# Kernel optimization log

Hardware: AMD Instinct MI355X
Metric: run time of the kernel (lower is better)

Reference implementation:

```python
import jax, jax.numpy as jnp
import numpy as np

D_MODEL = 1024
N_HEADS = 16
D_K = D_MODEL // N_HEADS
D_FF = 4096
EPS = 1e-5


def setup_inputs() -> dict:
    key = jax.random.key(0)
    ks = jax.random.split(key, 12)
    s = 1.0 / np.sqrt(D_MODEL)
    inp = {
        "x": jax.random.normal(ks[0], (2, 2048, D_MODEL), dtype=jnp.float32),
        "Wq": jax.random.normal(ks[1], (D_MODEL, D_MODEL), dtype=jnp.float32) * s,
        "Wk": jax.random.normal(ks[2], (D_MODEL, D_MODEL), dtype=jnp.float32) * s,
        "Wv": jax.random.normal(ks[3], (D_MODEL, D_MODEL), dtype=jnp.float32) * s,
        "Wo": jax.random.normal(ks[4], (D_MODEL, D_MODEL), dtype=jnp.float32) * s,
        "ln1_g": jnp.ones((D_MODEL,), jnp.float32),
        "ln1_b": jnp.zeros((D_MODEL,), jnp.float32),
        "ln2_g": jnp.ones((D_MODEL,), jnp.float32),
        "ln2_b": jnp.zeros((D_MODEL,), jnp.float32),
        "W1": jax.random.normal(ks[5], (D_MODEL, D_FF), dtype=jnp.float32) * s,
        "b1": jnp.zeros((D_FF,), jnp.float32),
        "W2": jax.random.normal(ks[6], (D_FF, D_MODEL), dtype=jnp.float32) * (1.0 / np.sqrt(D_FF)),
        "b2": jnp.zeros((D_MODEL,), jnp.float32),
    }
    return inp


def _layernorm(x, g, b):
    mu = jnp.mean(x, axis=-1, keepdims=True)
    var = jnp.mean(jnp.square(x - mu), axis=-1, keepdims=True)
    return (x - mu) / jnp.sqrt(var + EPS) * g + b


def _mha(x, Wq, Wk, Wv, Wo):
    B, S, D = x.shape
    def split_heads(t):
        return t.reshape(B, S, N_HEADS, D_K).transpose(0, 2, 1, 3)  # [B,H,S,Dk]
    Q = split_heads(x @ Wq)
    K = split_heads(x @ Wk)
    V = split_heads(x @ Wv)
    scores = jnp.einsum("bhsd,bhtd->bhst", Q, K) / np.sqrt(D_K)
    causal = jnp.tril(jnp.ones((S, S), dtype=bool))
    scores = jnp.where(causal, scores, -jnp.inf)
    weights = jax.nn.softmax(scores, axis=-1)
    out = jnp.einsum("bhst,bhtd->bhsd", weights, V)
    out = out.transpose(0, 2, 1, 3).reshape(B, S, D)
    return out @ Wo


def reference(x, Wq, Wk, Wv, Wo, ln1_g, ln1_b, ln2_g, ln2_b, W1, b1, W2, b2):
    # Pre-LN transformer block, dropout in eval mode (identity)
    x = x + _mha(_layernorm(x, ln1_g, ln1_b), Wq, Wk, Wv, Wo)
    h = _layernorm(x, ln2_g, ln2_b)
    ff = jax.nn.gelu(h @ W1 + b1, approximate=False) @ W2 + b2
    return x + ff
```

## Files before the change

kernel.cpp:

```cpp
#include <hip/hip_runtime.h>
#include <cstdint>
#include <cstddef>

#define DEV __device__ __forceinline__

typedef __attribute__((ext_vector_type(8))) __bf16 bf16x8;
typedef __attribute__((ext_vector_type(4))) float f32x4;
typedef __attribute__((ext_vector_type(8))) unsigned short u16x8;

typedef const __attribute__((address_space(1))) void gld_gv;
typedef __attribute__((address_space(3))) void gld_sv;

static constexpr int SEQ = 2048, BAT = 2, DM = 1024, DFF = 4096;
static constexpr int MT = BAT * SEQ;
static constexpr float LOG2E = 1.44269504088896340736f;
static constexpr float SM_SHIFT = 16.0f;

struct TrueC  { static constexpr bool value = true;  };
struct FalseC { static constexpr bool value = false; };

DEV unsigned short f2bf_bits(float f) {
    uint32_t u = __builtin_bit_cast(uint32_t, f);
    return (unsigned short)((u + 0x7FFFu + ((u >> 16) & 1u)) >> 16);
}

DEV void gload16(const void* g, void* s) {
    __builtin_amdgcn_global_load_lds((gld_gv*)g, (gld_sv*)s, 16, 0, 0);
}

__global__ __launch_bounds__(256) void wtrans_kernel(const float* __restrict__ W,
        unsigned short* __restrict__ WT, int K, int N, float scale)
{
    __shared__ float tile[64][65];
    const int k0 = blockIdx.x * 64, n0 = blockIdx.y * 64;
    const int t = threadIdx.x, r = t >> 6, c = t & 63;
    #pragma unroll
    for (int p = 0; p < 16; ++p)
        tile[p * 4 + r][c] = W[(size_t)(k0 + p * 4 + r) * N + n0 + c];
    __syncthreads();
    #pragma unroll
    for (int p = 0; p < 16; ++p)
        WT[(size_t)(n0 + p * 4 + r) * K + k0 + c] = f2bf_bits(tile[c][p * 4 + r] * scale);
}

__global__ __launch_bounds__(256) void ln_kernel(const float* __restrict__ x,
        const float* __restrict__ gw, const float* __restrict__ bw,
        unsigned short* __restrict__ y)
{
    const int row = blockIdx.x, t = threadIdx.x;
    const float* xr = x + (size_t)row * DM;
    float4 v = *(const float4*)(xr + t * 4);
    float s = v.x + v.y + v.z + v.w;
    float q = v.x * v.x + v.y * v.y + v.z * v.z + v.w * v.w;
    #pragma unroll
    for (int m = 1; m < 64; m <<= 1) { s += __shfl_xor(s, m); q += __shfl_xor(q, m); }
    __shared__ float red[8];
    const int w = t >> 6;
    if ((t & 63) == 0) { red[w] = s; red[4 + w] = q; }
    __syncthreads();
    s = red[0] + red[1] + red[2] + red[3];
    q = red[4] + red[5] + red[6] + red[7];
    const float mu = s * (1.0f / DM);
    const float rstd = rsqrtf(q * (1.0f / DM) - mu * mu + 1e-5f);
    float4 g4 = *(const float4*)(gw + t * 4);
    float4 b4 = *(const float4*)(bw + t * 4);
    short4 o;
    o.x = (short)f2bf_bits((v.x - mu) * rstd * g4.x + b4.x);
    o.y = (short)f2bf_bits((v.y - mu) * rstd * g4.y + b4.y);
    o.z = (short)f2bf_bits((v.z - mu) * rstd * g4.z + b4.z);
    o.w = (short)f2bf_bits((v.w - mu) * rstd * g4.w + b4.w);
    *(short4*)(y + (size_t)row * DM + t * 4) = o;
}

template<int EPI, int BM, int BN, int WVM, int WVN>
__global__ __launch_bounds__(WVM * WVN * 64, (BN == 64 ? 3 : 2)) void gemm_pipe(
    const unsigned short* __restrict__ A, const unsigned short* __restrict__ BT,
    void* __restrict__ Cp, const float* __restrict__ bias,
    const float* __restrict__ res, int Nsz, int Ksz, float scale)
{
    constexpr int NT = WVM * WVN * 64;
    constexpr int TOTCH = (BM + BN) * 8;
    constexpr int TL = TOTCH / NT;
    constexpr int MREP = BM / (WVM * 16);
    constexpr int WMR = MREP * 16;
    __shared__ alignas(16) unsigned short lds[2][(BM + BN) * 64];

    const int t = threadIdx.x, l = t & 63, w = t >> 6;
    const int wm = w / WVN, wn = w % WVN;
    const int lr = l & 15, lg = l >> 4;
    const int bm = blockIdx.x, bn = blockIdx.y;

    f32x4 acc[MREP][4] = {};

    const int nk = Ksz / 64;

    auto STAGE = [&](int tile, char* slot) {
        const int k0 = tile * 64;
        #pragma unroll
        for (int p = 0; p < TL; ++p) {
            const int ci = t + p * NT;
            const bool isA = ci < BM * 8;
            const int rr = (isA ? ci : ci - BM * 8) >> 3;
            const int cc = ci & 7;
            const unsigned short* srow = isA
                ? A + (size_t)(bm * BM + rr) * Ksz
                : BT + (size_t)(bn * BN + rr) * Ksz;
            gload16(srow + k0 + ((cc ^ (rr & 7)) << 3), slot + ci * 16);
        }
    };

    STAGE(0, (char*)lds[0]);
    STAGE(1, (char*)lds[1]);

    for (int kt = 0; kt < nk; ++kt) {
        char* slot = (char*)lds[kt & 1];
        const char* la = slot;
        const char* lb = slot + BM * 128;
        if (kt + 1 < nk) {
            if constexpr (TL == 8) asm volatile("s_waitcnt vmcnt(8)" ::: "memory");
            else                   asm volatile("s_waitcnt vmcnt(6)" ::: "memory");
        } else {
            asm volatile("s_waitcnt vmcnt(0)" ::: "memory");
        }
        __builtin_amdgcn_s_barrier();
        __builtin_amdgcn_sched_barrier(0);

        __builtin_amdgcn_s_setprio(1);
        #pragma unroll
        for (int ks = 0; ks < 2; ++ks) {
            bf16x8 af[MREP], bfr[4];
            #pragma unroll
            for (int i = 0; i < MREP; ++i) {
                const int ra = wm * WMR + i * 16 + lr;
                af[i] = *(const bf16x8*)(la + (ra * 8 + ((ks * 4 + lg) ^ (ra & 7))) * 16);
            }
            #pragma unroll
            for (int i = 0; i < 4; ++i) {
                const int rb_ = wn * 64 + i * 16 + lr;
                bfr[i] = *(const bf16x8*)(lb + (rb_ * 8 + ((ks * 4 + lg) ^ (rb_ & 7))) * 16);
            }
            #pragma unroll
            for (int mb = 0; mb < MREP; ++mb)
                #pragma unroll
                for (int nb = 0; nb < 4; ++nb) {
                    if (EPI == 4)
                        acc[mb][nb] = __builtin_amdgcn_mfma_f32_16x16x32_bf16(
                            bfr[nb], af[mb], acc[mb][nb], 0, 0, 0);
                    else
                        acc[mb][nb] = __builtin_amdgcn_mfma_f32_16x16x32_bf16(
                            af[mb], bfr[nb], acc[mb][nb], 0, 0, 0);
                }
        }
        __builtin_amdgcn_s_setprio(0);
        __builtin_amdgcn_s_barrier();
        if (kt + 2 < nk) STAGE(kt + 2, slot);
    }

    const int rb = bm * BM + wm * WMR, cb = bn * BN + wn * 64;
    #pragma unroll
    for (int mb = 0; mb < MREP; ++mb)
        #pragma unroll
        for (int nb = 0; nb < 4; ++nb)
            #pragma unroll
            for (int r = 0; r < 4; ++r) {
                float v = acc[mb][nb][r];
                if (EPI == 4) {
                    const int xrow = rb + mb * 16 + lr;
                    const int feat = cb + nb * 16 + lg * 4 + r;
                    const int bb = xrow >> 11, s = xrow & (SEQ - 1);
                    ((unsigned short*)Cp)[((size_t)bb * DM + feat) * SEQ + s] = f2bf_bits(v);
                    continue;
                }
                const int row = rb + mb * 16 + lg * 4 + r;
                const int col = cb + nb * 16 + lr;
                const size_t idx = (size_t)row * Nsz + col;
                if (EPI == 0) {
                    ((unsigned short*)Cp)[idx] = f2bf_bits(v * scale);
                } else if (EPI == 1) {
                    ((float*)Cp)[idx] = v + res[idx];
                } else if (EPI == 2) {
                    float xx = v + bias[col];
                    ((unsigned short*)Cp)[idx] =
                        f2bf_bits(0.5f * xx * (1.0f + erff(xx * 0.70710678118654752f)));
                } else {
                    ((float*)Cp)[idx] = v + bias[col] + res[idx];
                }
            }
}

template<int P>
DEV void phase8_mfma(const char* base, int wm, int lr, int lg,
                     const bf16x8 (&bfr)[2][4], f32x4 (&acc)[8][4]) {
    bf16x8 af[2][2];
    #pragma unroll
    for (int ks = 0; ks < 2; ++ks)
        #pragma unroll
        for (int m = 0; m < 2; ++m) {
            const int ra = wm * 128 + P * 32 + m * 16 + lr;
            af[ks][m] = *(const bf16x8*)(base + (ra * 8 + ((ks * 4 + lg) ^ (ra & 7))) * 16);
        }
    __builtin_amdgcn_s_barrier();
    __builtin_amdgcn_s_setprio(1);
    #pragma unroll
    for (int ks = 0; ks < 2; ++ks)
        #pragma unroll
        for (int m = 0; m < 2; ++m)
            #pragma unroll
            for (int nb = 0; nb < 4; ++nb)
                acc[P * 2 + m][nb] = __builtin_amdgcn_mfma_f32_16x16x32_bf16(
                    af[ks][m], bfr[ks][nb], acc[P * 2 + m][nb], 0, 0, 0);
    __builtin_amdgcn_s_setprio(0);
}

template<int EPI>
__global__ __launch_bounds__(512, 2) void gemm_8ph(
    const unsigned short* __restrict__ A, const unsigned short* __restrict__ BT,
    void* __restrict__ Cp, const float* __restrict__ bias,
    const float* __restrict__ res, int Nsz, int Ksz, float scale)
{
    __shared__ alignas(16) unsigned short lds[2][32768];
    const int t = threadIdx.x, l = t & 63, w = t >> 6;
    const int wm = w >> 2, wn = w & 3;
    const int lr = l & 15, lg = l >> 4;
    const int bm = blockIdx.x, bn = blockIdx.y;

    f32x4 acc[8][4] = {};
    const int nk = Ksz / 64;

    const unsigned short* Ab = A + (size_t)(bm * 256) * Ksz;
    const unsigned short* Bb = BT + (size_t)(bn * 256) * Ksz;

    auto stage = [&](int tile, int region) {
        char* base = (char*)lds[tile & 1];
        const int k0 = tile * 64;
        #pragma unroll
        for (int j = 0; j < 2; ++j) {
            const int ci = t + j * 512;
            const int rr = ci >> 3, c = ci & 7;
            int row; const unsigned short* src; int dchunk;
            if (region == 0)      { row = rr;                          src = Bb; dchunk = 2048 + row * 8 + c; }
            else if (region == 1) { row = 128 + rr;                    src = Bb; dchunk = 2048 + row * 8 + c; }
            else if (region == 2) { row = (rr < 64 ? rr : rr + 64);    src = Ab; dchunk = row * 8 + c; }
            else                  { row = 64 + (rr < 64 ? rr : rr + 64); src = Ab; dchunk = row * 8 + c; }
            gload16(src + (size_t)row * Ksz + k0 + ((c ^ (row & 7)) << 3),
                    base + dchunk * 16);
        }
    };

    stage(0, 0); stage(0, 1); stage(0, 2); stage(0, 3);
    stage(1, 0); stage(1, 1); stage(1, 2);
    asm volatile("s_waitcnt vmcnt(6)" ::: "memory");
    __builtin_amdgcn_s_barrier();
    __builtin_amdgcn_sched_barrier(0);

    bf16x8 bfr[2][4];
    for (int kt = 0; kt < nk; ++kt) {
        const char* base = (const char*)lds[kt & 1];
        if (kt + 1 < nk) stage(kt + 1, 3);
        #pragma unroll
        for (int ks = 0; ks < 2; ++ks)
            #pragma unroll
            for (int nb = 0; nb < 4; ++nb) {
                const int rb_ = wn * 64 + nb * 16 + lr;
                bfr[ks][nb] = *(const bf16x8*)(base
                    + (2048 + rb_ * 8 + ((ks * 4 + lg) ^ (rb_ & 7))) * 16);
            }
        phase8_mfma<0>(base, wm, lr, lg, bfr, acc);
        __builtin_amdgcn_s_barrier();
        if (kt + 2 < nk) stage(kt + 2, 0);
        phase8_mfma<1>(base, wm, lr, lg, bfr, acc);
        __builtin_amdgcn_s_barrier();
        if (kt + 2 < nk) stage(kt + 2, 1);
        phase8_mfma<2>(base, wm, lr, lg, bfr, acc);
        __builtin_amdgcn_s_barrier();
        if (kt + 2 < nk) stage(kt + 2, 2);
        phase8_mfma<3>(base, wm, lr, lg, bfr, acc);
        if (kt + 2 < nk) asm volatile("s_waitcnt vmcnt(6)" ::: "memory");
        else             asm volatile("s_waitcnt vmcnt(0)" ::: "memory");
        __builtin_amdgcn_s_barrier();
        __builtin_amdgcn_sched_barrier(0);
    }

    const int rb = bm * 256 + wm * 128, cb = bn * 256 + wn * 64;
    #pragma unroll
    for (int mb = 0; mb < 8; ++mb)
        #pragma unroll
        for (int nb = 0; nb < 4; ++nb)
            #pragma unroll
            for (int r = 0; r < 4; ++r) {
                float v = acc[mb][nb][r];
                const int row = rb + mb * 16 + lg * 4 + r;
                const int col = cb + nb * 16 + lr;
                const size_t idx = (size_t)row * Nsz + col;
                if (EPI == 2) {
                    const float xx = v + bias[col];
                    const float tq = xx * xx;
                    const float u = xx * fmaf(tq, 0.044715f, 1.0f);
                    const float e = exp2f(u * -2.30220795f);
                    ((unsigned short*)Cp)[idx] =
                        f2bf_bits(xx * __builtin_amdgcn_rcpf(1.0f + e));
                } else if (EPI == 0) {
                    ((unsigned short*)Cp)[idx] = f2bf_bits(v * scale);
                } else {
                    ((float*)Cp)[idx] = v + bias[col] + res[idx];
                }
            }
}

__global__ __launch_bounds__(512, 2) void attn_kernel(
    const unsigned short* __restrict__ QKg, const unsigned short* __restrict__ VTg,
    unsigned short* __restrict__ Og)
{
    __shared__ alignas(16) unsigned short ldsK[2][128 * 64];
    __shared__ alignas(16) unsigned short ldsVT[2][64 * 128];
    const int t = threadIdx.x, l = t & 63, w = t >> 6;
    const int lr = l & 15, lg = l >> 4;
    const int qtA = blockIdx.x, qtB = 15 - qtA;
    const int bh = blockIdx.y;
    const int b = bh >> 4, h = bh & 15;
    const unsigned short* Qbase = QKg + (size_t)b * SEQ * 2048 + h * 64;
    const unsigned short* Kbase = Qbase + 1024;
    const unsigned short* Vbase = VTg + (size_t)b * DM * SEQ + (size_t)(h * 64) * SEQ;

    const int wq0A = qtA * 128 + w * 16, qrowA = wq0A + lr;
    const int wq0B = qtB * 128 + w * 16, qrowB = wq0B + lr;
    bf16x8 qfA[2], qfB[2];
    #pragma unroll
    for (int ks = 0; ks < 2; ++ks) {
        qfA[ks] = *(const bf16x8*)(Qbase + (size_t)qrowA * 2048 + ks * 32 + lg * 8);
        qfB[ks] = *(const bf16x8*)(Qbase + (size_t)qrowB * 2048 + ks * 32 + lg * 8);
    }

    f32x4 oaccA[4] = {}, oaccB[4] = {};
    f32x4 laccA = {}, laccB = {};
    bf16x8 onesv;
    #pragma unroll
    for (int i = 0; i < 8; ++i) onesv[i] = (__bf16)1.0f;

    const int kci[2] = { t, t + 512 };
    const int nkt = qtB + 1;

    #pragma unroll
    for (int p = 0; p < 2; ++p) {
        const int ci = kci[p];
        const int kr = ci >> 3, kc = (ci & 7) ^ (kr & 7);
        gload16(Kbase + (size_t)kr * 2048 + kc * 8, (char*)ldsK[0] + ci * 16);
        const int vr = ci >> 4, vc = (ci & 15) ^ (vr & 15);
        gload16(Vbase + (size_t)vr * SEQ + vc * 8, (char*)ldsVT[0] + ci * 16);
    }
    asm volatile("s_waitcnt vmcnt(0)" ::: "memory");
    __builtin_amdgcn_s_barrier();

    for (int kt = 0; kt < nkt; ++kt) {
        const int cur = kt & 1;
        if (kt + 1 < nkt) {
            #pragma unroll
            for (int p = 0; p < 2; ++p) {
                const int ci = kci[p];
                const int kr = ci >> 3, kc = (ci & 7) ^ (kr & 7);
                gload16(Kbase + (size_t)((kt + 1) * 128 + kr) * 2048 + kc * 8,
                        (char*)ldsK[cur ^ 1] + ci * 16);
                const int vr = ci >> 4, vc = (ci & 15) ^ (vr & 15);
                gload16(Vbase + (size_t)vr * SEQ + (kt + 1) * 128 + vc * 8,
                        (char*)ldsVT[cur ^ 1] + ci * 16);
            }
        }
        const char* lk = (const char*)ldsK[cur];
        const char* lv = (const char*)ldsVT[cur];
        const int kt0 = kt * 128;

        auto run_softmax = [&](f32x4 (&st)[8], int qrow, bool diag, bf16x8 (&pa)[4]) {
            if (diag) {
                #pragma unroll
                for (int mb = 0; mb < 8; ++mb)
                    #pragma unroll
                    for (int r = 0; r < 4; ++r)
                        if (kt0 + mb * 16 + lg * 4 + r > qrow) st[mb][r] = -1e30f;
            }
            #pragma unroll
            for (int mb = 0; mb < 8; ++mb)
                #pragma unroll
                for (int r = 0; r < 4; ++r)
                    st[mb][r] = exp2f(st[mb][r]);
            #pragma unroll
            for (int ks = 0; ks < 4; ++ks)
                #pragma unroll
                for (int j = 0; j < 4; ++j) {
                    pa[ks][j]     = (__bf16)st[2 * ks][j];
                    pa[ks][j + 4] = (__bf16)st[2 * ks + 1][j];
                }
        };

        auto iter_body = [&](auto DOA) {
            constexpr bool doA = DOA.value;
            f32x4 stA[8], stB[8];
            #pragma unroll
            for (int mb = 0; mb < 8; ++mb)
                #pragma unroll
                for (int r = 0; r < 4; ++r) { stA[mb][r] = -SM_SHIFT; stB[mb][r] = -SM_SHIFT; }
            __builtin_amdgcn_s_setprio(1);
            #pragma unroll
            for (int ks = 0; ks < 2; ++ks)
                #pragma unroll
                for (int mb = 0; mb < 8; ++mb) {
                    bf16x8 kf = *(const bf16x8*)(lk + (mb * 16 + lr) * 128
                                                 + (((ks * 4 + lg) ^ (lr & 7)) * 16));
                    if constexpr (doA)
                        stA[mb] = __builtin_amdgcn_mfma_f32_16x16x32_bf16(kf, qfA[ks], stA[mb], 0, 0, 0);
                    stB[mb] = __builtin_amdgcn_mfma_f32_16x16x32_bf16(kf, qfB[ks], stB[mb], 0, 0, 0);
                }
            __builtin_amdgcn_s_setprio(0);

            bf16x8 paA[4], paB[4];
            if constexpr (doA)
                run_softmax(stA, qrowA, kt == qtA, paA);
            run_softmax(stB, qrowB, kt == qtB, paB);

            __builtin_amdgcn_s_setprio(1);
            #pragma unroll
            for (int ks = 0; ks < 4; ++ks) {
                #pragma unroll
                for (int nb = 0; nb < 4; ++nb) {
                    const int n = nb * 16 + lr;
                    union { bf16x8 v; uint64_t d[2]; } vb;
                    vb.d[0] = *(const uint64_t*)(lv + n * 256
                                + (((4 * ks + (lg >> 1)) ^ (n & 15)) * 16) + 8 * (lg & 1));
                    vb.d[1] = *(const uint64_t*)(lv + n * 256
                                + (((4 * ks + 2 + (lg >> 1)) ^ (n & 15)) * 16) + 8 * (lg & 1));
                    if constexpr (doA)
                        oaccA[nb] = __builtin_amdgcn_mfma_f32_16x16x32_bf16(paA[ks], vb.v, oaccA[nb], 0, 0, 0);
                    oaccB[nb] = __builtin_amdgcn_mfma_f32_16x16x32_bf16(paB[ks], vb.v, oaccB[nb], 0, 0, 0);
                }
                if constexpr (doA)
                    laccA = __builtin_amdgcn_mfma_f32_16x16x32_bf16(paA[ks], onesv, laccA, 0, 0, 0);
                laccB = __builtin_amdgcn_mfma_f32_16x16x32_bf16(paB[ks], onesv, laccB, 0, 0, 0);
            }
            __builtin_amdgcn_s_setprio(0);
        };

        if (kt <= qtA) iter_body(TrueC{}); else iter_body(FalseC{});

        asm volatile("s_waitcnt vmcnt(0)" ::: "memory");
        __builtin_amdgcn_s_barrier();
    }

    unsigned short* Obase = Og + (size_t)b * SEQ * DM + h * 64;
    #pragma unroll
    for (int j = 0; j < 4; ++j) {
        const float invA = 1.0f / laccA[j];
        const float invB = 1.0f / laccB[j];
        const int rowA = wq0A + lg * 4 + j;
        const int rowB = wq0B + lg * 4 + j;
        #pragma unroll
        for (int nb = 0; nb < 4; ++nb) {
            Obase[(size_t)rowA * DM + nb * 16 + lr] = f2bf_bits(oaccA[nb][j] * invA);
            Obase[(size_t)rowB * DM + nb * 16 + lr] = f2bf_bits(oaccB[nb][j] * invB);
        }
    }
}

extern "C" void kernel_launch(void* const* d_in, const int* in_sizes, int n_in,
                              void* d_out, int out_size, void* d_ws, size_t ws_size,
                              hipStream_t stream) {
    (void)in_sizes; (void)n_in; (void)out_size; (void)ws_size;
    const float* x    = (const float*)d_in[0];
    const float* Wq   = (const float*)d_in[1];
    const float* Wk   = (const float*)d_in[2];
    const float* Wv   = (const float*)d_in[3];
    const float* Wo   = (const float*)d_in[4];
    const float* ln1g = (const float*)d_in[5];
    const float* ln1b = (const float*)d_in[6];
    const float* ln2g = (const float*)d_in[7];
    const float* ln2b = (const float*)d_in[8];
    const float* W1   = (const float*)d_in[9];
    const float* b1   = (const float*)d_in[10];
    const float* W2   = (const float*)d_in[11];
    const float* b2   = (const float*)d_in[12];
    float* out = (float*)d_out;

    char* ws = (char*)d_ws;
    const size_t MB = 1ull << 20;
    unsigned short* xn1   = (unsigned short*)(ws + 0 * MB);
    unsigned short* QKb   = (unsigned short*)(ws + 8 * MB);
    unsigned short* VTg   = (unsigned short*)(ws + 24 * MB);
    unsigned short* ffa   = (unsigned short*)(ws + 0 * MB);
    unsigned short* attno = (unsigned short*)(ws + 32 * MB);
    float*          x2    = (float*)(ws + 40 * MB);
    unsigned short* h2    = (unsigned short*)(ws + 56 * MB);
    unsigned short* WqkT  = (unsigned short*)(ws + 64 * MB);
    unsigned short* WvT   = (unsigned short*)(ws + 68 * MB);
    unsigned short* WoT   = (unsigned short*)(ws + 70 * MB);
    unsigned short* W1T   = (unsigned short*)(ws + 72 * MB);
    unsigned short* W2T   = (unsigned short*)(ws + 80 * MB);

    dim3 blk(256);
    wtrans_kernel<<<dim3(16, 16), blk, 0, stream>>>(Wq, WqkT, DM, DM, 0.125f * LOG2E);
    wtrans_kernel<<<dim3(16, 16), blk, 0, stream>>>(Wk, WqkT + DM * DM, DM, DM, 1.0f);
    wtrans_kernel<<<dim3(16, 16), blk, 0, stream>>>(Wv, WvT, DM, DM, 1.0f);
    wtrans_kernel<<<dim3(16, 16), blk, 0, stream>>>(Wo, WoT, DM, DM, 1.0f);
    wtrans_kernel<<<dim3(16, 64), blk, 0, stream>>>(W1, W1T, DM, DFF, 1.0f);
    wtrans_kernel<<<dim3(64, 16), blk, 0, stream>>>(W2, W2T, DFF, DM, 1.0f);

    ln_kernel<<<dim3(MT), blk, 0, stream>>>(x, ln1g, ln1b, xn1);

    gemm_pipe<0, 128, 256, 2, 4><<<dim3(32, 8), dim3(512), 0, stream>>>(
        xn1, WqkT, QKb, nullptr, nullptr, 2048, DM, 1.0f);
    gemm_pipe<4, 128, 64, 4, 1><<<dim3(32, 16), blk, 0, stream>>>(
        xn1, WvT, VTg, nullptr, nullptr, DM, DM, 1.0f);

    attn_kernel<<<dim3(8, 32), dim3(512), 0, stream>>>(QKb, VTg, attno);

    gemm_pipe<1, 128, 64, 4, 1><<<dim3(32, 16), blk, 0, stream>>>(
        attno, WoT, x2, nullptr, x, DM, DM, 1.0f);

    ln_kernel<<<dim3(MT), blk, 0, stream>>>(x2, ln2g, ln2b, h2);

    gemm_8ph<2><<<dim3(16, 16), dim3(512), 0, stream>>>(
        h2, W1T, ffa, b1, nullptr, DFF, DM, 1.0f);
    gemm_pipe<3, 128, 64, 4, 1><<<dim3(32, 16), blk, 0, stream>>>(
        ffa, W2T, out, b2, x2, DM, DFF, 1.0f);
}
```

Measured before the change: 226.4 us.

## Store K and V in MFMA fragment order so attention loads are contiguous

The QK projection epilogue now writes K into a per-head tile layout that matches the MFMA operand fragments, and the V projection epilogue writes V in a similar fragment order. The attention kernel can then copy contiguous chunks into LDS and read each operand with a single linear 16-byte load per lane, with no XOR swizzle or split 8-byte loads. This removes address math and gives fully coalesced global loads in the attention inner loop. The cost is scattered, poorly coalesced 2-byte stores in the projection GEMM epilogues, and possible LDS bank conflicts now that the swizzle is gone.

```diff
diff --git a/kernel.cpp b/kernel.cpp
--- a/kernel.cpp
+++ b/kernel.cpp
@@ -6,7 +6,6 @@
 
 typedef __attribute__((ext_vector_type(8))) __bf16 bf16x8;
 typedef __attribute__((ext_vector_type(4))) float f32x4;
-typedef __attribute__((ext_vector_type(8))) unsigned short u16x8;
 
 typedef const __attribute__((address_space(1))) void gld_gv;
 typedef __attribute__((address_space(3))) void gld_sv;
@@ -167,12 +166,31 @@
                 if (EPI == 4) {
                     const int xrow = rb + mb * 16 + lr;
                     const int feat = cb + nb * 16 + lg * 4 + r;
-                    const int bb = xrow >> 11, s = xrow & (SEQ - 1);
-                    ((unsigned short*)Cp)[((size_t)bb * DM + feat) * SEQ + s] = f2bf_bits(v);
+                    const int bb = xrow >> 11, sl = xrow & (SEQ - 1);
+                    const int hh = feat >> 6, n = feat & 63;
+                    const int nbf = n >> 4, lrf = n & 15;
+                    const int ksg = sl >> 5, lgf = (sl & 15) >> 2;
+                    const int half = (sl >> 4) & 1, j = sl & 3;
+                    ((unsigned short*)Cp)[((size_t)(bb * 16 + hh) * 256 + ksg * 4 + nbf) * 512
+                        + (lgf * 16 + lrf) * 8 + half * 4 + j] = f2bf_bits(v);
                     continue;
                 }
                 const int row = rb + mb * 16 + lg * 4 + r;
                 const int col = cb + nb * 16 + lr;
+                if (EPI == 5) {
+                    if (col < 1024) {
+                        ((unsigned short*)Cp)[(size_t)row * 1024 + col] = f2bf_bits(v);
+                    } else {
+                        const int bb = row >> 11, sl = row & (SEQ - 1);
+                        const int hh = (col >> 6) & 15, d = col & 63;
+                        const int ktf = sl >> 7, mbf = (sl & 127) >> 4, lrf = sl & 15;
+                        const int ksf = d >> 5, lgf = (d & 31) >> 3, j2 = d & 7;
+                        unsigned short* Kf = (unsigned short*)(uintptr_t)bias;
+                        Kf[((((size_t)(bb * 16 + hh) * 16 + ktf) * 8 + mbf) * 2 + ksf) * 512
+                           + (lgf * 16 + lrf) * 8 + j2] = f2bf_bits(v);
+                    }
+                    continue;
+                }
                 const size_t idx = (size_t)row * Nsz + col;
                 if (EPI == 0) {
                     ((unsigned short*)Cp)[idx] = f2bf_bits(v * scale);
@@ -308,8 +326,8 @@
 }
 
 __global__ __launch_bounds__(512, 2) void attn_kernel(
-    const unsigned short* __restrict__ QKg, const unsigned short* __restrict__ VTg,
-    unsigned short* __restrict__ Og)
+    const unsigned short* __restrict__ Qg, const unsigned short* __restrict__ Kfg,
+    const unsigned short* __restrict__ Vfg, unsigned short* __restrict__ Og)
 {
     __shared__ alignas(16) unsigned short ldsK[2][128 * 64];
     __shared__ alignas(16) unsigned short ldsVT[2][64 * 128];
@@ -318,17 +336,17 @@
     const int qtA = blockIdx.x, qtB = 15 - qtA;
     const int bh = blockIdx.y;
     const int b = bh >> 4, h = bh & 15;
-    const unsigned short* Qbase = QKg + (size_t)b * SEQ * 2048 + h * 64;
-    const unsigned short* Kbase = Qbase + 1024;
-    const unsigned short* Vbase = VTg + (size_t)b * DM * SEQ + (size_t)(h * 64) * SEQ;
+    const unsigned short* Qbase = Qg + (size_t)b * SEQ * 1024 + h * 64;
+    const unsigned short* Kbase = Kfg + (size_t)bh * 131072;
+    const unsigned short* Vbase = Vfg + (size_t)bh * 131072;
 
     const int wq0A = qtA * 128 + w * 16, qrowA = wq0A + lr;
     const int wq0B = qtB * 128 + w * 16, qrowB = wq0B + lr;
     bf16x8 qfA[2], qfB[2];
     #pragma unroll
     for (int ks = 0; ks < 2; ++ks) {
-        qfA[ks] = *(const bf16x8*)(Qbase + (size_t)qrowA * 2048 + ks * 32 + lg * 8);
-        qfB[ks] = *(const bf16x8*)(Qbase + (size_t)qrowB * 2048 + ks * 32 + lg * 8);
+        qfA[ks] = *(const bf16x8*)(Qbase + (size_t)qrowA * 1024 + ks * 32 + lg * 8);
+        qfB[ks] = *(const bf16x8*)(Qbase + (size_t)qrowB * 1024 + ks * 32 + lg * 8);
     }
 
     f32x4 oaccA[4] = {}, oaccB[4] = {};
@@ -337,16 +355,14 @@
     #pragma unroll
     for (int i = 0; i < 8; ++i) onesv[i] = (__bf16)1.0f;
 
-    const int kci[2] = { t, t + 512 };
+    const int lby = l * 16;
     const int nkt = qtB + 1;
 
     #pragma unroll
     for (int p = 0; p < 2; ++p) {
-        const int ci = kci[p];
-        const int kr = ci >> 3, kc = (ci & 7) ^ (kr & 7);
-        gload16(Kbase + (size_t)kr * 2048 + kc * 8, (char*)ldsK[0] + ci * 16);
-        const int vr = ci >> 4, vc = (ci & 15) ^ (vr & 15);
-        gload16(Vbase + (size_t)vr * SEQ + vc * 8, (char*)ldsVT[0] + ci * 16);
+        const int ci = t + p * 512;
+        gload16(Kbase + (size_t)ci * 8, (char*)ldsK[0] + ci * 16);
+        gload16(Vbase + (size_t)ci * 8, (char*)ldsVT[0] + ci * 16);
     }
     asm volatile("s_waitcnt vmcnt(0)" ::: "memory");
     __builtin_amdgcn_s_barrier();
@@ -356,12 +372,10 @@
         if (kt + 1 < nkt) {
             #pragma unroll
             for (int p = 0; p < 2; ++p) {
-                const int ci = kci[p];
-                const int kr = ci >> 3, kc = (ci & 7) ^ (kr & 7);
-                gload16(Kbase + (size_t)((kt + 1) * 128 + kr) * 2048 + kc * 8,
+                const int ci = t + p * 512;
+                gload16(Kbase + (size_t)((kt + 1) * 1024 + ci) * 8,
                         (char*)ldsK[cur ^ 1] + ci * 16);
-                const int vr = ci >> 4, vc = (ci & 15) ^ (vr & 15);
-                gload16(Vbase + (size_t)vr * SEQ + (kt + 1) * 128 + vc * 8,
+                gload16(Vbase + (size_t)((kt + 1) * 1024 + ci) * 8,
                         (char*)ldsVT[cur ^ 1] + ci * 16);
             }
         }
@@ -403,8 +417,7 @@
             for (int ks = 0; ks < 2; ++ks)
                 #pragma unroll
                 for (int mb = 0; mb < 8; ++mb) {
-                    bf16x8 kf = *(const bf16x8*)(lk + (mb * 16 + lr) * 128
-                                                 + (((ks * 4 + lg) ^ (lr & 7)) * 16));
+                    bf16x8 kf = *(const bf16x8*)(lk + (mb * 2 + ks) * 1024 + lby);
                     if constexpr (doA)
                         stA[mb] = __builtin_amdgcn_mfma_f32_16x16x32_bf16(kf, qfA[ks], stA[mb], 0, 0, 0);
                     stB[mb] = __builtin_amdgcn_mfma_f32_16x16x32_bf16(kf, qfB[ks], stB[mb], 0, 0, 0);
@@ -421,15 +434,10 @@
             for (int ks = 0; ks < 4; ++ks) {
                 #pragma unroll
                 for (int nb = 0; nb < 4; ++nb) {
-                    const int n = nb * 16 + lr;
-                    union { bf16x8 v; uint64_t d[2]; } vb;
-                    vb.d[0] = *(const uint64_t*)(lv + n * 256
-                                + (((4 * ks + (lg >> 1)) ^ (n & 15)) * 16) + 8 * (lg & 1));
-                    vb.d[1] = *(const uint64_t*)(lv + n * 256
-                                + (((4 * ks + 2 + (lg >> 1)) ^ (n & 15)) * 16) + 8 * (lg & 1));
+                    bf16x8 vbv = *(const bf16x8*)(lv + (ks * 4 + nb) * 1024 + lby);
                     if constexpr (doA)
-                        oaccA[nb] = __builtin_amdgcn_mfma_f32_16x16x32_bf16(paA[ks], vb.v, oaccA[nb], 0, 0, 0);
-                    oaccB[nb] = __builtin_amdgcn_mfma_f32_16x16x32_bf16(paB[ks], vb.v, oaccB[nb], 0, 0, 0);
+                        oaccA[nb] = __builtin_amdgcn_mfma_f32_16x16x32_bf16(paA[ks], vbv, oaccA[nb], 0, 0, 0);
+                    oaccB[nb] = __builtin_amdgcn_mfma_f32_16x16x32_bf16(paB[ks], vbv, oaccB[nb], 0, 0, 0);
                 }
                 if constexpr (doA)
                     laccA = __builtin_amdgcn_mfma_f32_16x16x32_bf16(paA[ks], onesv, laccA, 0, 0, 0);
@@ -481,8 +489,9 @@
     char* ws = (char*)d_ws;
     const size_t MB = 1ull << 20;
     unsigned short* xn1   = (unsigned short*)(ws + 0 * MB);
-    unsigned short* QKb   = (unsigned short*)(ws + 8 * MB);
-    unsigned short* VTg   = (unsigned short*)(ws + 24 * MB);
+    unsigned short* Qb    = (unsigned short*)(ws + 8 * MB);
+    unsigned short* Kf    = (unsigned short*)(ws + 16 * MB);
+    unsigned short* Vf    = (unsigned short*)(ws + 24 * MB);
     unsigned short* ffa   = (unsigned short*)(ws + 0 * MB);
     unsigned short* attno = (unsigned short*)(ws + 32 * MB);
     float*          x2    = (float*)(ws + 40 * MB);
@@ -503,12 +512,12 @@
 
     ln_kernel<<<dim3(MT), blk, 0, stream>>>(x, ln1g, ln1b, xn1);
 
-    gemm_pipe<0, 128, 256, 2, 4><<<dim3(32, 8), dim3(512), 0, stream>>>(
-        xn1, WqkT, QKb, nullptr, nullptr, 2048, DM, 1.0f);
+    gemm_pipe<5, 128, 256, 2, 4><<<dim3(32, 8), dim3(512), 0, stream>>>(
+        xn1, WqkT, Qb, (const float*)Kf, nullptr, 2048, DM, 1.0f);
     gemm_pipe<4, 128, 64, 4, 1><<<dim3(32, 16), blk, 0, stream>>>(
-        xn1, WvT, VTg, nullptr, nullptr, DM, DM, 1.0f);
-
-    attn_kernel<<<dim3(8, 32), dim3(512), 0, stream>>>(QKb, VTg, attno);
+        xn1, WvT, Vf, nullptr, nullptr, DM, DM, 1.0f);
+
+    attn_kernel<<<dim3(8, 32), dim3(512), 0, stream>>>(Qb, Kf, Vf, attno);
 
     gemm_pipe<1, 128, 64, 4, 1><<<dim3(32, 16), blk, 0, stream>>>(
         attno, WoT, x2, nullptr, x, DM, DM, 1.0f);
```

After: 227.0 us. About the same (+0.3%).
